# Kernel optimization log

Hardware: AMD Instinct MI355X
Metric: run time of the kernel (lower is better)

Reference implementation:

```python
import jax, jax.numpy as jnp
import numpy as np

S, T, B, IN, H, O = 64, 32, 512, 66, 1024, 1024  # S == max_length


def _gru_cell(x, h, Wih, Whh, bih, bhh):
    # PyTorch GRU cell: gates ordered (r, z, n)
    gi = x @ Wih.T + bih            # [B, 3H]
    gh = h @ Whh.T + bhh            # [B, 3H]
    ir, iz, inn = jnp.split(gi, 3, axis=1)
    hr, hz, hn = jnp.split(gh, 3, axis=1)
    r = jax.nn.sigmoid(ir + hr)
    z = jax.nn.sigmoid(iz + hz)
    n = jnp.tanh(inn + r * hn)
    return (1.0 - z) * n + z * h


def setup_inputs() -> dict:
    key = jax.random.key(0)
    ks = jax.random.split(key, 20)
    s = 0.02
    return {
        "input_tensor": jax.random.normal(ks[0], (S, B, IN), jnp.float32),
        "target_tensor": jax.random.normal(ks[1], (T, B, H), jnp.float32),
        # encoder GRU
        "enc_Wih": jax.random.normal(ks[2], (3 * H, IN), jnp.float32) * s,
        "enc_Whh": jax.random.normal(ks[3], (3 * H, H), jnp.float32) * s,
        "enc_bih": jax.random.normal(ks[4], (3 * H,), jnp.float32) * s,
        "enc_bhh": jax.random.normal(ks[5], (3 * H,), jnp.float32) * s,
        # attention: Linear(2H -> max_length)
        "attn_W": jax.random.normal(ks[6], (S, 2 * H), jnp.float32) * s,
        "attn_b": jax.random.normal(ks[7], (S,), jnp.float32) * s,
        # attn_combine: Linear(2H -> H)
        "comb_W": jax.random.normal(ks[8], (H, 2 * H), jnp.float32) * s,
        "comb_b": jax.random.normal(ks[9], (H,), jnp.float32) * s,
        # decoder GRU
        "dec_Wih": jax.random.normal(ks[10], (3 * H, H), jnp.float32) * s,
        "dec_Whh": jax.random.normal(ks[11], (3 * H, H), jnp.float32) * s,
        "dec_bih": jax.random.normal(ks[12], (3 * H,), jnp.float32) * s,
        "dec_bhh": jax.random.normal(ks[13], (3 * H,), jnp.float32) * s,
        # output: Linear(H -> O)
        "out_W": jax.random.normal(ks[14], (O, H), jnp.float32) * s,
        "out_b": jax.random.normal(ks[15], (O,), jnp.float32) * s,
    }


def reference(input_tensor, target_tensor, enc_Wih, enc_Whh, enc_bih, enc_bhh,
              attn_W, attn_b, comb_W, comb_b, dec_Wih, dec_Whh, dec_bih,
              dec_bhh, out_W, out_b):
    batch = input_tensor.shape[1]
    h0 = jnp.zeros((batch, enc_Whh.shape[1]), input_tensor.dtype)

    # ---- encoder GRU over time ----
    def enc_step(h, x):
        h2 = _gru_cell(x, h, enc_Wih, enc_Whh, enc_bih, enc_bhh)
        return h2, h2

    enc_h, enc_out = jax.lax.scan(enc_step, h0, input_tensor)  # enc_out: [S, B, H]

    # ---- attention decoder, teacher forcing; loop t = 1..T-1 uses target[t-1] ----
    def dec_step(h, x):
        aw = jax.nn.softmax(jnp.concatenate([x, h], axis=1) @ attn_W.T + attn_b,
                            axis=1)                              # [B, S]
        ctx = jnp.einsum('bl,lbh->bh', aw, enc_out)              # [B, H]
        comb = jax.nn.relu(jnp.concatenate([x, ctx], axis=1) @ comb_W.T + comb_b)
        h2 = _gru_cell(comb, h, dec_Wih, dec_Whh, dec_bih, dec_bhh)
        out = jax.nn.log_softmax(h2 @ out_W.T + out_b, axis=1)   # [B, O]
        return h2, out

    _, outs = jax.lax.scan(dec_step, enc_h, target_tensor[:-1])
    # original overwrites `outputs` every step -> only last step survives
    return outs[-1]
```

## Files before the change

### kernel.cpp

```cpp
#include <hip/hip_runtime.h>
#include <hip/hip_bf16.h>
#include <math.h>

#define S_LEN 64
#define T_LEN 32
#define BATCH 512
#define IN_DIM 66
#define INP 128
#define H_DIM 1024
#define O_DIM 1024
#define H3 3072

typedef __attribute__((ext_vector_type(8))) short short8;
typedef __attribute__((ext_vector_type(4))) float f32x4;
typedef __attribute__((ext_vector_type(4))) unsigned short us4;

__device__ __forceinline__ unsigned short f2b(float f) {
    union { float f; unsigned u; } x; x.f = f;
    unsigned r = x.u + 0x7FFF + ((x.u >> 16) & 1);
    return (unsigned short)(r >> 16);
}
__device__ __forceinline__ float b2f(unsigned short s) {
    union { unsigned u; float f; } x; x.u = ((unsigned)s) << 16;
    return x.f;
}
__device__ __forceinline__ void gll16(const void* g, const void* l) {
    __builtin_amdgcn_global_load_lds(
        (const __attribute__((address_space(1))) unsigned int*)g,
        (__attribute__((address_space(3))) unsigned int*)l, 16, 0, 0);
}

template<int TM, int TN>
__global__ __launch_bounds__(256) void gemm_k(
    const unsigned short* __restrict__ A, int lda,
    const unsigned short* __restrict__ W, int ldw,
    const float* __restrict__ bias,
    const float* __restrict__ addf, const unsigned short* __restrict__ addb,
    int ldadd,
    float* __restrict__ Cf,
    unsigned short* __restrict__ Cb, int ldc,
    int K, int flags)
{
    constexpr int IF = TM / 16;
    constexpr int JF = TN / 64;
    constexpr int NW = TN / 4;
    constexpr int CA = TM * 4;
    constexpr int CW = TN * 4;
    __shared__ __align__(16) unsigned short As[TM * 32];
    __shared__ __align__(16) unsigned short Bs[TN * 32];

    const int bm = blockIdx.y * TM;
    const int bn = blockIdx.x * TN;
    const int t = threadIdx.x;
    const int lane = t & 63;
    const int wv = t >> 6;
    const int ln = lane & 15;
    const int quad = lane >> 4;

    f32x4 acc[IF][JF];
    #pragma unroll
    for (int i = 0; i < IF; i++)
        #pragma unroll
        for (int j = 0; j < JF; j++) {
            f32x4 z = {0.f, 0.f, 0.f, 0.f};
            acc[i][j] = z;
        }

    for (int k0 = 0; k0 < K; k0 += 32) {
        if constexpr (CA >= 256) {
            #pragma unroll
            for (int j = 0; j < CA / 256; j++) {
                int ch = j * 256 + t;
                gll16(A + (size_t)(bm + (ch >> 2)) * lda + k0 + (ch & 3) * 8,
                      (const char*)As + (j * 4 + wv) * 1024);
            }
        } else {
            if (t < CA)
                gll16(A + (size_t)(bm + (t >> 2)) * lda + k0 + (t & 3) * 8,
                      (const char*)As + wv * 1024);
        }
        if constexpr (CW >= 256) {
            #pragma unroll
            for (int j = 0; j < CW / 256; j++) {
                int ch = j * 256 + t;
                gll16(W + (size_t)(bn + (ch >> 2)) * ldw + k0 + (ch & 3) * 8,
                      (const char*)Bs + (j * 4 + wv) * 1024);
            }
        } else {
            if (t < CW)
                gll16(W + (size_t)(bn + (t >> 2)) * ldw + k0 + (t & 3) * 8,
                      (const char*)Bs + wv * 1024);
        }
        __syncthreads();
        short8 af[IF], bf[JF];
        #pragma unroll
        for (int i = 0; i < IF; i++)
            af[i] = *(const short8*)&As[(i * 16 + ln) * 32 + quad * 8];
        #pragma unroll
        for (int j = 0; j < JF; j++)
            bf[j] = *(const short8*)&Bs[(wv * NW + j * 16 + ln) * 32 + quad * 8];
        #pragma unroll
        for (int i = 0; i < IF; i++)
            #pragma unroll
            for (int j = 0; j < JF; j++)
                acc[i][j] = __builtin_amdgcn_mfma_f32_16x16x32_bf16(
                    af[i], bf[j], acc[i][j], 0, 0, 0);
        __syncthreads();
    }

    #pragma unroll
    for (int i = 0; i < IF; i++) {
        #pragma unroll
        for (int j = 0; j < JF; j++) {
            #pragma unroll
            for (int r = 0; r < 4; r++) {
                int m = bm + i * 16 + quad * 4 + r;
                int n = bn + wv * NW + j * 16 + ln;
                float v = acc[i][j][r];
                if (flags & 1) v += bias[n];
                if (flags & 2) v += addf[(size_t)m * ldadd + n];
                if (flags & 4) v += b2f(addb[(size_t)m * ldadd + n]);
                if (flags & 8) v = fmaxf(v, 0.f);
                if (flags & 16) Cf[(size_t)m * ldc + n] = v;
                if (flags & 32) Cb[(size_t)m * ldc + n] = f2b(v);
            }
        }
    }
}

__device__ __forceinline__ void gru_tile(
    const unsigned short* __restrict__ A, int lda,
    const unsigned short* __restrict__ W, int ldw, int kb,
    unsigned short* As_g, unsigned short* Ws_g,
    int bm, int bn, int gt, int gwv, int ln, int quad,
    f32x4 (&accR)[2], f32x4 (&accZ)[2], f32x4 (&accN)[2])
{
    {
        int s = gt >> 7, r = (gt >> 2) & 31, c = gt & 3;
        gll16(A + (size_t)(bm + r) * lda + kb + s * 32 + c * 8,
              (const char*)As_g + gwv * 1024);
    }
    #pragma unroll
    for (int j = 0; j < 6; j++) {
        int ch = j * 256 + gt;
        int g2 = ch >> 9, ch2 = ch & 511;
        int s = ch2 >> 8, r = (ch2 >> 2) & 63, c = ch2 & 3;
        gll16(W + (size_t)(g2 * H_DIM + bn + r) * ldw + kb + s * 32 + c * 8,
              (const char*)Ws_g + j * 4096 + gwv * 1024);
    }
    __syncthreads();
    #pragma unroll
    for (int sub = 0; sub < 2; sub++) {
        short8 a[2], bw[3];
        #pragma unroll
        for (int i = 0; i < 2; i++)
            a[i] = *(const short8*)&As_g[sub * 1024 + (i * 16 + ln) * 32 + quad * 8];
        #pragma unroll
        for (int g = 0; g < 3; g++)
            bw[g] = *(const short8*)&Ws_g[g * 4096 + sub * 2048 + (gwv * 16 + ln) * 32 + quad * 8];
        #pragma unroll
        for (int i = 0; i < 2; i++) {
            accR[i] = __builtin_amdgcn_mfma_f32_16x16x32_bf16(a[i], bw[0], accR[i], 0, 0, 0);
            accZ[i] = __builtin_amdgcn_mfma_f32_16x16x32_bf16(a[i], bw[1], accZ[i], 0, 0, 0);
            accN[i] = __builtin_amdgcn_mfma_f32_16x16x32_bf16(a[i], bw[2], accN[i], 0, 0, 0);
        }
    }
    __syncthreads();
}

__global__ __launch_bounds__(512) void gru_gemm(
    const unsigned short* __restrict__ A0, int lda0,
    const unsigned short* __restrict__ W0, int ldw0, int K0,
    const unsigned short* __restrict__ A1,
    const unsigned short* __restrict__ W1,
    const float* __restrict__ bih, const float* __restrict__ bhh,
    const float* __restrict__ hf_in, float* __restrict__ hf_out,
    unsigned short* __restrict__ hb_out, unsigned short* __restrict__ slot)
{
    __shared__ __align__(16) unsigned short As2[2][2 * 32 * 32];
    __shared__ __align__(16) unsigned short Ws2[2][3 * 2 * 64 * 32];
    const int bm = blockIdx.y * 32;
    const int bn = blockIdx.x * 64;
    const int t = threadIdx.x;
    const int wg = t >> 8;
    const int gt = t & 255;
    const int lane = t & 63;
    const int gwv = gt >> 6;
    const int ln = lane & 15;
    const int quad = lane >> 4;

    unsigned short* As_g = As2[wg];
    unsigned short* Ws_g = Ws2[wg];

    f32x4 accR[2], accZ[2], accN0[2], accN1[2];
    #pragma unroll
    for (int i = 0; i < 2; i++) {
        f32x4 z = {0.f, 0.f, 0.f, 0.f};
        accR[i] = z; accZ[i] = z; accN0[i] = z; accN1[i] = z;
    }

    const int half0 = K0 >> 1;
    for (int k0 = 0; k0 < half0; k0 += 64)
        gru_tile(A0, lda0, W0, ldw0, wg * half0 + k0, As_g, Ws_g,
                 bm, bn, gt, gwv, ln, quad, accR, accZ, accN0);
    for (int k0 = 0; k0 < 512; k0 += 64)
        gru_tile(A1, H_DIM, W1, H_DIM, wg * 512 + k0, As_g, Ws_g,
                 bm, bn, gt, gwv, ln, quad, accR, accZ, accN1);

    float* red = (float*)Ws2;
    const int rb = (gwv * 64 + lane) * 33;
    if (wg == 1) {
        #pragma unroll
        for (int i = 0; i < 2; i++)
            #pragma unroll
            for (int r = 0; r < 4; r++) {
                red[rb + i * 4 + r]      = accR[i][r];
                red[rb + 8 + i * 4 + r]  = accZ[i][r];
                red[rb + 16 + i * 4 + r] = accN0[i][r];
                red[rb + 24 + i * 4 + r] = accN1[i][r];
            }
    }
    __syncthreads();
    if (wg == 0) {
        #pragma unroll
        for (int i = 0; i < 2; i++)
            #pragma unroll
            for (int r = 0; r < 4; r++) {
                accR[i][r]  += red[rb + i * 4 + r];
                accZ[i][r]  += red[rb + 8 + i * 4 + r];
                accN0[i][r] += red[rb + 16 + i * 4 + r];
                accN1[i][r] += red[rb + 24 + i * 4 + r];
            }
        const int n = bn + gwv * 16 + ln;
        const float br = bih[n] + bhh[n];
        const float bz = bih[H_DIM + n] + bhh[H_DIM + n];
        const float bi_n = bih[2 * H_DIM + n];
        const float bh_n = bhh[2 * H_DIM + n];
        #pragma unroll
        for (int i = 0; i < 2; i++) {
            #pragma unroll
            for (int r = 0; r < 4; r++) {
                const int m = bm + i * 16 + quad * 4 + r;
                const size_t idx = (size_t)m * H_DIM + n;
                float rg = 1.f / (1.f + __expf(-(accR[i][r] + br)));
                float zg = 1.f / (1.f + __expf(-(accZ[i][r] + bz)));
                float av = accN0[i][r] + bi_n + rg * (accN1[i][r] + bh_n);
                float e2 = __expf(-2.f * fabsf(av));
                float th = (1.f - e2) / (1.f + e2);
                th = av < 0.f ? -th : th;
                float o = (1.f - zg) * th + zg * hf_in[idx];
                hf_out[idx] = o;
                unsigned short ob = f2b(o);
                hb_out[idx] = ob;
                if (slot) slot[idx] = ob;
            }
        }
    }
}

__global__ __launch_bounds__(256) void attn_ctx(
    const unsigned short* __restrict__ hb,
    const unsigned short* __restrict__ wAhT,
    const unsigned short* __restrict__ attnx_t,
    const unsigned short* __restrict__ encb,
    unsigned short* __restrict__ ctx)
{
    __shared__ float hf[H_DIM];
    __shared__ float part[4][S_LEN];
    __shared__ float awl[S_LEN];
    const int b = blockIdx.x, t = threadIdx.x;
    {
        us4 u = *(const us4*)(hb + ((size_t)b << 10) + t * 4);
        #pragma unroll
        for (int j = 0; j < 4; j++) hf[t * 4 + j] = b2f(u[j]);
    }
    __syncthreads();
    {
        const int c = t & 63, ks = (t >> 6) * 256;
        float s = 0.f;
        #pragma unroll 8
        for (int k = 0; k < 256; k++)
            s += hf[ks + k] * b2f(wAhT[(size_t)(ks + k) * S_LEN + c]);
        part[t >> 6][c] = s;
    }
    __syncthreads();
    if (t < 64) {
        float v = part[0][t] + part[1][t] + part[2][t] + part[3][t]
                + b2f(attnx_t[b * S_LEN + t]);
        float m = v;
        #pragma unroll
        for (int off = 32; off; off >>= 1) m = fmaxf(m, __shfl_xor(m, off));
        float e = __expf(v - m);
        float ss = e;
        #pragma unroll
        for (int off = 32; off; off >>= 1) ss += __shfl_xor(ss, off);
        awl[t] = e / ss;
    }
    __syncthreads();
    const int hq = t * 4;
    float s0 = 0.f, s1 = 0.f, s2 = 0.f, s3 = 0.f;
    #pragma unroll 4
    for (int l = 0; l < S_LEN; l++) {
        us4 u = *(const us4*)(encb + (((size_t)l * BATCH + b) << 10) + hq);
        float w = awl[l];
        s0 += w * b2f(u[0]); s1 += w * b2f(u[1]);
        s2 += w * b2f(u[2]); s3 += w * b2f(u[3]);
    }
    us4 o; o[0] = f2b(s0); o[1] = f2b(s1); o[2] = f2b(s2); o[3] = f2b(s3);
    *(us4*)(ctx + ((size_t)b << 10) + hq) = o;
}

__global__ void cvt_w4(const float* __restrict__ src, int ld,
                       unsigned short* __restrict__ dst, int rows, int cols)
{
    int idx = blockIdx.x * blockDim.x + threadIdx.x;
    int total4 = rows * cols / 4;
    if (idx >= total4) return;
    int e = idx * 4;
    int r = e / cols, c = e - r * cols;
    const float* s = src + (size_t)r * ld + c;
    us4 o;
    #pragma unroll
    for (int j = 0; j < 4; j++) o[j] = f2b(s[j]);
    *(us4*)(dst + e) = o;
}

__global__ void cvt_plain4(const float* __restrict__ src,
                           unsigned short* __restrict__ dst, int total4)
{
    int idx = blockIdx.x * blockDim.x + threadIdx.x;
    if (idx >= total4) return;
    f32x4 v = *(const f32x4*)(src + (size_t)idx * 4);
    us4 o;
    #pragma unroll
    for (int j = 0; j < 4; j++) o[j] = f2b(v[j]);
    *(us4*)(dst + (size_t)idx * 4) = o;
}

__global__ void cvt_pad(const float* __restrict__ src, int scols,
                        unsigned short* __restrict__ dst, int dcols, int total)
{
    int idx = blockIdx.x * blockDim.x + threadIdx.x;
    if (idx >= total) return;
    int r = idx / dcols, c = idx - r * dcols;
    dst[idx] = (c < scols) ? f2b(src[(size_t)r * scols + c]) : (unsigned short)0;
}

__global__ void cvt_attT(const float* __restrict__ attn_W,
                         unsigned short* __restrict__ dst)
{
    int idx = blockIdx.x * blockDim.x + threadIdx.x;
    if (idx >= S_LEN * H_DIM) return;
    int k = idx >> 6, c = idx & 63;
    dst[idx] = f2b(attn_W[(size_t)c * 2 * H_DIM + H_DIM + k]);
}

__global__ void log_softmax1024(float* __restrict__ x)
{
    __shared__ float red[256];
    float* xr = x + (size_t)blockIdx.x * O_DIM;
    int t = threadIdx.x;
    float m = -1e30f;
    for (int i = t; i < O_DIM; i += 256) m = fmaxf(m, xr[i]);
    red[t] = m; __syncthreads();
    for (int s2 = 128; s2 > 0; s2 >>= 1) {
        if (t < s2) red[t] = fmaxf(red[t], red[t + s2]);
        __syncthreads();
    }
    m = red[0];
    __syncthreads();
    float s = 0.f;
    for (int i = t; i < O_DIM; i += 256) s += expf(xr[i] - m);
    red[t] = s; __syncthreads();
    for (int s2 = 128; s2 > 0; s2 >>= 1) {
        if (t < s2) red[t] += red[t + s2];
        __syncthreads();
    }
    float lse = m + logf(red[0]);
    __syncthreads();
    for (int i = t; i < O_DIM; i += 256) xr[i] = xr[i] - lse;
}

extern "C" void kernel_launch(void* const* d_in, const int* in_sizes, int n_in,
                              void* d_out, int out_size, void* d_ws, size_t ws_size,
                              hipStream_t stream)
{
    const float* input   = (const float*)d_in[0];
    const float* target  = (const float*)d_in[1];
    const float* enc_Wih = (const float*)d_in[2];
    const float* enc_Whh = (const float*)d_in[3];
    const float* enc_bih = (const float*)d_in[4];
    const float* enc_bhh = (const float*)d_in[5];
    const float* attn_W  = (const float*)d_in[6];
    const float* attn_b  = (const float*)d_in[7];
    const float* comb_W  = (const float*)d_in[8];
    const float* comb_b  = (const float*)d_in[9];
    const float* dec_Wih = (const float*)d_in[10];
    const float* dec_Whh = (const float*)d_in[11];
    const float* dec_bih = (const float*)d_in[12];
    const float* dec_bhh = (const float*)d_in[13];
    const float* out_W   = (const float*)d_in[14];
    const float* out_b   = (const float*)d_in[15];
    float* out = (float*)d_out;

    char* p = (char*)d_ws;
    auto alloc = [&](size_t bytes) {
        char* r = p; p += (bytes + 255) & ~(size_t)255; return r;
    };
    unsigned short* wWhh  = (unsigned short*)alloc((size_t)H3 * H_DIM * 2);
    unsigned short* wDih  = (unsigned short*)alloc((size_t)H3 * H_DIM * 2);
    unsigned short* wDhh  = (unsigned short*)alloc((size_t)H3 * H_DIM * 2);
    unsigned short* wCc   = (unsigned short*)alloc((size_t)H_DIM * H_DIM * 2);
    unsigned short* wCx   = (unsigned short*)alloc((size_t)H_DIM * H_DIM * 2);
    unsigned short* wO    = (unsigned short*)alloc((size_t)O_DIM * H_DIM * 2);
    unsigned short* wAhT  = (unsigned short*)alloc((size_t)H_DIM * S_LEN * 2);
    unsigned short* wAx   = (unsigned short*)alloc((size_t)S_LEN * H_DIM * 2);
    unsigned short* wIhp  = (unsigned short*)alloc((size_t)H3 * INP * 2);
    unsigned short* xbp   = (unsigned short*)alloc((size_t)S_LEN * BATCH * INP * 2);
    unsigned short* encb  = (unsigned short*)alloc((size_t)S_LEN * BATCH * H_DIM * 2);
    unsigned short* combx = (unsigned short*)alloc((size_t)(T_LEN - 1) * BATCH * H_DIM * 2);
    unsigned short* attnx = (unsigned short*)alloc((size_t)(T_LEN - 1) * BATCH * S_LEN * 2);
    float*          h     = (float*)alloc((size_t)BATCH * H_DIM * 4);
    unsigned short* hbA   = (unsigned short*)alloc((size_t)BATCH * H_DIM * 2);
    unsigned short* hbB   = (unsigned short*)alloc((size_t)BATCH * H_DIM * 2);
    unsigned short* ctx   = (unsigned short*)alloc((size_t)BATCH * H_DIM * 2);
    unsigned short* comb  = (unsigned short*)alloc((size_t)BATCH * H_DIM * 2);
    unsigned short* targetb = encb;

    const dim3 blk(256);

    hipMemsetAsync(h,   0, (size_t)BATCH * H_DIM * 4, stream);
    hipMemsetAsync(hbA, 0, (size_t)BATCH * H_DIM * 2, stream);

    cvt_w4<<<(H3 * H_DIM / 4 + 255) / 256, blk, 0, stream>>>(enc_Whh, H_DIM, wWhh, H3, H_DIM);
    cvt_w4<<<(H3 * H_DIM / 4 + 255) / 256, blk, 0, stream>>>(dec_Wih, H_DIM, wDih, H3, H_DIM);
    cvt_w4<<<(H3 * H_DIM / 4 + 255) / 256, blk, 0, stream>>>(dec_Whh, H_DIM, wDhh, H3, H_DIM);
    cvt_w4<<<(H_DIM * H_DIM / 4 + 255) / 256, blk, 0, stream>>>(comb_W + H_DIM, 2 * H_DIM, wCc, H_DIM, H_DIM);
    cvt_w4<<<(H_DIM * H_DIM / 4 + 255) / 256, blk, 0, stream>>>(comb_W, 2 * H_DIM, wCx, H_DIM, H_DIM);
    cvt_w4<<<(O_DIM * H_DIM / 4 + 255) / 256, blk, 0, stream>>>(out_W, H_DIM, wO, O_DIM, H_DIM);
    cvt_w4<<<(S_LEN * H_DIM / 4 + 255) / 256, blk, 0, stream>>>(attn_W, 2 * H_DIM, wAx, S_LEN, H_DIM);
    cvt_attT<<<(S_LEN * H_DIM + 255) / 256, blk, 0, stream>>>(attn_W, wAhT);
    cvt_pad<<<((S_LEN * BATCH * INP) + 255) / 256, blk, 0, stream>>>(
        input, IN_DIM, xbp, INP, S_LEN * BATCH * INP);
    cvt_pad<<<((H3 * INP) + 255) / 256, blk, 0, stream>>>(
        enc_Wih, IN_DIM, wIhp, INP, H3 * INP);
    cvt_plain4<<<((T_LEN * BATCH * H_DIM / 4) + 255) / 256, blk, 0, stream>>>(
        target, targetb, T_LEN * BATCH * H_DIM / 4);

    const int MT = (T_LEN - 1) * BATCH;
    gemm_k<64, 64><<<dim3(1, MT / 64), blk, 0, stream>>>(
        targetb, H_DIM, wAx, H_DIM, attn_b,
        nullptr, nullptr, 0, nullptr, attnx, S_LEN, H_DIM, 1 | 32);
    gemm_k<128, 128><<<dim3(H_DIM / 128, MT / 128), blk, 0, stream>>>(
        targetb, H_DIM, wCx, H_DIM, comb_b,
        nullptr, nullptr, 0, nullptr, combx, H_DIM, H_DIM, 1 | 32);

    const dim3 grid_gru(H_DIM / 64, BATCH / 32);
    const dim3 blk512(512);
    unsigned short* hcur = hbA;
    unsigned short* hnxt = hbB;

    for (int s = 0; s < S_LEN; s++) {
        gru_gemm<<<grid_gru, blk512, 0, stream>>>(
            xbp + (size_t)s * BATCH * INP, INP, wIhp, INP, INP,
            hcur, wWhh, enc_bih, enc_bhh, h, h, hnxt,
            encb + (size_t)s * BATCH * H_DIM);
        unsigned short* tmp = hcur; hcur = hnxt; hnxt = tmp;
    }

    for (int t = 0; t < T_LEN - 1; t++) {
        attn_ctx<<<BATCH, blk, 0, stream>>>(
            hcur, wAhT, attnx + (size_t)t * BATCH * S_LEN, encb, ctx);
        gemm_k<32, 64><<<dim3(H_DIM / 64, BATCH / 32), blk, 0, stream>>>(
            ctx, H_DIM, wCc, H_DIM, nullptr,
            nullptr, combx + (size_t)t * BATCH * H_DIM, H_DIM,
            nullptr, comb, H_DIM, H_DIM, 4 | 8 | 32);
        gru_gemm<<<grid_gru, blk512, 0, stream>>>(
            comb, H_DIM, wDih, H_DIM, H_DIM,
            hcur, wDhh, dec_bih, dec_bhh, h, h, hnxt, nullptr);
        unsigned short* tmp = hcur; hcur = hnxt; hnxt = tmp;
    }

    gemm_k<32, 64><<<dim3(O_DIM / 64, BATCH / 32), blk, 0, stream>>>(
        hcur, H_DIM, wO, H_DIM, out_b,
        nullptr, nullptr, 0, out, nullptr, O_DIM, H_DIM, 1 | 16);
    log_softmax1024<<<BATCH, blk, 0, stream>>>(out);
}
```

Baseline: 3.145 ms.

## Double-buffer LDS tiles in GEMM and GRU GEMM kernels

Both the generic MFMA GEMM and the fused GRU GEMM now use two shared-memory buffers per operand tile. The global-to-LDS loads for the next K tile are issued before the MFMAs on the current tile, and there is one barrier per iteration instead of two. The aim is to hide global load latency behind matrix-core work in the recurrent steps. In exchange, LDS use roughly doubles, which may lower occupancy in gru_gemm, and the overlap depends on how the compiler places waitcnt before the barrier.

```diff
diff --git a/kernel.cpp b/kernel.cpp
--- a/kernel.cpp
+++ b/kernel.cpp
@@ -46,8 +46,8 @@
     constexpr int NW = TN / 4;
     constexpr int CA = TM * 4;
     constexpr int CW = TN * 4;
-    __shared__ __align__(16) unsigned short As[TM * 32];
-    __shared__ __align__(16) unsigned short Bs[TN * 32];
+    __shared__ __align__(16) unsigned short As[2][TM * 32];
+    __shared__ __align__(16) unsigned short Bs[2][TN * 32];
 
     const int bm = blockIdx.y * TM;
     const int bn = blockIdx.x * TN;
@@ -66,45 +66,52 @@
             acc[i][j] = z;
         }
 
-    for (int k0 = 0; k0 < K; k0 += 32) {
+    auto stage = [&](int buf, int k0) {
         if constexpr (CA >= 256) {
             #pragma unroll
             for (int j = 0; j < CA / 256; j++) {
                 int ch = j * 256 + t;
                 gll16(A + (size_t)(bm + (ch >> 2)) * lda + k0 + (ch & 3) * 8,
-                      (const char*)As + (j * 4 + wv) * 1024);
+                      (const char*)As[buf] + (j * 4 + wv) * 1024);
             }
         } else {
             if (t < CA)
                 gll16(A + (size_t)(bm + (t >> 2)) * lda + k0 + (t & 3) * 8,
-                      (const char*)As + wv * 1024);
+                      (const char*)As[buf] + wv * 1024);
         }
         if constexpr (CW >= 256) {
             #pragma unroll
             for (int j = 0; j < CW / 256; j++) {
                 int ch = j * 256 + t;
                 gll16(W + (size_t)(bn + (ch >> 2)) * ldw + k0 + (ch & 3) * 8,
-                      (const char*)Bs + (j * 4 + wv) * 1024);
+                      (const char*)Bs[buf] + (j * 4 + wv) * 1024);
             }
         } else {
             if (t < CW)
                 gll16(W + (size_t)(bn + (t >> 2)) * ldw + k0 + (t & 3) * 8,
-                      (const char*)Bs + wv * 1024);
+                      (const char*)Bs[buf] + wv * 1024);
         }
-        __syncthreads();
+    };
+
+    const int nt = K >> 5;
+    stage(0, 0);
+    __syncthreads();
+    for (int i = 0; i < nt; ++i) {
+        const int cur = i & 1;
+        if (i + 1 < nt) stage(cur ^ 1, (i + 1) << 5);
         short8 af[IF], bf[JF];
         #pragma unroll
-        for (int i = 0; i < IF; i++)
-            af[i] = *(const short8*)&As[(i * 16 + ln) * 32 + quad * 8];
+        for (int ii = 0; ii < IF; ii++)
+            af[ii] = *(const short8*)&As[cur][(ii * 16 + ln) * 32 + quad * 8];
         #pragma unroll
         for (int j = 0; j < JF; j++)
-            bf[j] = *(const short8*)&Bs[(wv * NW + j * 16 + ln) * 32 + quad * 8];
-        #pragma unroll
-        for (int i = 0; i < IF; i++)
+            bf[j] = *(const short8*)&Bs[cur][(wv * NW + j * 16 + ln) * 32 + quad * 8];
+        #pragma unroll
+        for (int ii = 0; ii < IF; ii++)
             #pragma unroll
             for (int j = 0; j < JF; j++)
-                acc[i][j] = __builtin_amdgcn_mfma_f32_16x16x32_bf16(
-                    af[i], bf[j], acc[i][j], 0, 0, 0);
+                acc[ii][j] = __builtin_amdgcn_mfma_f32_16x16x32_bf16(
+                    af[ii], bf[j], acc[ii][j], 0, 0, 0);
         __syncthreads();
     }
 
@@ -128,12 +135,11 @@
     }
 }
 
-__device__ __forceinline__ void gru_tile(
+__device__ __forceinline__ void gru_stage(
     const unsigned short* __restrict__ A, int lda,
     const unsigned short* __restrict__ W, int ldw, int kb,
     unsigned short* As_g, unsigned short* Ws_g,
-    int bm, int bn, int gt, int gwv, int ln, int quad,
-    f32x4 (&accR)[2], f32x4 (&accZ)[2], f32x4 (&accN)[2])
+    int bm, int bn, int gt, int gwv)
 {
     {
         int s = gt >> 7, r = (gt >> 2) & 31, c = gt & 3;
@@ -148,7 +154,13 @@
         gll16(W + (size_t)(g2 * H_DIM + bn + r) * ldw + kb + s * 32 + c * 8,
               (const char*)Ws_g + j * 4096 + gwv * 1024);
     }
-    __syncthreads();
+}
+
+__device__ __forceinline__ void gru_compute(
+    const unsigned short* As_g, const unsigned short* Ws_g,
+    int gwv, int ln, int quad,
+    f32x4 (&accR)[2], f32x4 (&accZ)[2], f32x4 (&accN)[2])
+{
     #pragma unroll
     for (int sub = 0; sub < 2; sub++) {
         short8 a[2], bw[3];
@@ -165,7 +177,6 @@
             accN[i] = __builtin_amdgcn_mfma_f32_16x16x32_bf16(a[i], bw[2], accN[i], 0, 0, 0);
         }
     }
-    __syncthreads();
 }
 
 __global__ __launch_bounds__(512) void gru_gemm(
@@ -177,8 +188,8 @@
     const float* __restrict__ hf_in, float* __restrict__ hf_out,
     unsigned short* __restrict__ hb_out, unsigned short* __restrict__ slot)
 {
-    __shared__ __align__(16) unsigned short As2[2][2 * 32 * 32];
-    __shared__ __align__(16) unsigned short Ws2[2][3 * 2 * 64 * 32];
+    __shared__ __align__(16) unsigned short As2[2][2][2 * 32 * 32];
+    __shared__ __align__(16) unsigned short Ws2[2][2][3 * 2 * 64 * 32];
     const int bm = blockIdx.y * 32;
     const int bn = blockIdx.x * 64;
     const int t = threadIdx.x;
@@ -189,9 +200,6 @@
     const int ln = lane & 15;
     const int quad = lane >> 4;
 
-    unsigned short* As_g = As2[wg];
-    unsigned short* Ws_g = Ws2[wg];
-
     f32x4 accR[2], accZ[2], accN0[2], accN1[2];
     #pragma unroll
     for (int i = 0; i < 2; i++) {
@@ -200,12 +208,27 @@
     }
 
     const int half0 = K0 >> 1;
-    for (int k0 = 0; k0 < half0; k0 += 64)
-        gru_tile(A0, lda0, W0, ldw0, wg * half0 + k0, As_g, Ws_g,
-                 bm, bn, gt, gwv, ln, quad, accR, accZ, accN0);
-    for (int k0 = 0; k0 < 512; k0 += 64)
-        gru_tile(A1, H_DIM, W1, H_DIM, wg * 512 + k0, As_g, Ws_g,
-                 bm, bn, gt, gwv, ln, quad, accR, accZ, accN1);
+    const int nt0 = half0 >> 6;
+    const int nt = nt0 + 8;
+
+    auto stg = [&](int i, int buf) {
+        const unsigned short* A; int lda; const unsigned short* W; int ldw; int kb;
+        if (i < nt0) { A = A0; lda = lda0; W = W0; ldw = ldw0; kb = wg * half0 + (i << 6); }
+        else         { A = A1; lda = H_DIM; W = W1; ldw = H_DIM; kb = wg * 512 + ((i - nt0) << 6); }
+        gru_stage(A, lda, W, ldw, kb, As2[wg][buf], Ws2[wg][buf], bm, bn, gt, gwv);
+    };
+
+    stg(0, 0);
+    __syncthreads();
+    for (int i = 0; i < nt; ++i) {
+        const int cur = i & 1;
+        if (i + 1 < nt) stg(i + 1, cur ^ 1);
+        if (i < nt0)
+            gru_compute(As2[wg][cur], Ws2[wg][cur], gwv, ln, quad, accR, accZ, accN0);
+        else
+            gru_compute(As2[wg][cur], Ws2[wg][cur], gwv, ln, quad, accR, accZ, accN1);
+        __syncthreads();
+    }
 
     float* red = (float*)Ws2;
     const int rb = (gwv * 64 + lane) * 33;
```

Result: no change. 3.089 ms (-1.8%).
